# Kernel optimization log

Measured on AMD Instinct MI355X. Metric: run time of the kernel, lower is better.

Reference implementation:

```python
import jax, jax.numpy as jnp
import numpy as np


def _mlp(h, W1, b1, W2, b2):
    # Linear -> ReLU -> Linear
    h = jax.nn.relu(h @ W1 + b1)
    return h @ W2 + b2


def setup_inputs() -> dict:
    key = jax.random.key(0)
    ks = jax.random.split(key, 8)
    N, E, DN, DE, H, O = 50000, 800000, 128, 64, 256, 128
    DIN = DN + DE  # 192
    s1 = 1.0 / np.sqrt(DIN)
    s2 = 1.0 / np.sqrt(H)
    return {
        "x": jax.random.normal(ks[0], (N, DN), dtype=jnp.float32),
        "edge_index": jax.random.randint(ks[1], (2, E), 0, N, dtype=jnp.int32),
        "edge_attr": jax.random.normal(ks[2], (E, DE), dtype=jnp.float32),
        "W1_out": jax.random.normal(ks[3], (DIN, H), dtype=jnp.float32) * s1,
        "b1_out": jnp.zeros((H,), dtype=jnp.float32),
        "W2_out": jax.random.normal(ks[4], (H, O), dtype=jnp.float32) * s2,
        "b2_out": jnp.zeros((O,), dtype=jnp.float32),
        "W1_in": jax.random.normal(ks[5], (DIN, H), dtype=jnp.float32) * s1,
        "b1_in": jnp.zeros((H,), dtype=jnp.float32),
        "W2_in": jax.random.normal(ks[6], (H, O), dtype=jnp.float32) * s2,
        "b2_in": jnp.zeros((O,), dtype=jnp.float32),
    }


def reference(x, edge_index, edge_attr, W1_out, b1_out, W2_out, b2_out,
              W1_in, b1_in, W2_in, b2_in):
    N = x.shape[0]
    row, col = edge_index[0], edge_index[1]
    # Shared gather + concat: [E, d_node + d_edge]
    msg_in = jnp.concatenate([x[col], edge_attr], axis=1)

    # flow_out: edges with row < col. Compute MLP densely, zero masked edges,
    # then scatter-sum -> identical math to masked gather + scatter-sum.
    m_out = (row < col).astype(x.dtype)[:, None]
    flow_out = _mlp(msg_in, W1_out, b1_out, W2_out, b2_out) * m_out
    flow_out = jax.ops.segment_sum(flow_out, row, num_segments=N)

    # flow_in: edges with row > col
    m_in = (row > col).astype(x.dtype)[:, None]
    flow_in = _mlp(msg_in, W1_in, b1_in, W2_in, b2_in) * m_in
    flow_in = jax.ops.segment_sum(flow_in, row, num_segments=N)

    return jnp.concatenate((flow_in, flow_out), axis=1)  # [N, 2*O]
```

## Files before the change

### kernel.cpp

```cpp
#include <hip/hip_runtime.h>
#include <hip/hip_bf16.h>

typedef __attribute__((ext_vector_type(8))) short short8;
typedef __attribute__((ext_vector_type(4))) float f32x4;

#define DN   128
#define DE   64
#define DIN  192
#define HID  256
#define OUTD 128
#define TE   64
#define MSG_LD 200
#define H_LD   264

static __device__ __forceinline__ unsigned short f2b(float f) {
    unsigned int u = __float_as_uint(f);
    u += 0x7fffu + ((u >> 16) & 1u);
    return (unsigned short)(u >> 16);
}

__global__ void pack_all_kernel(const float* __restrict__ W1o, const float* __restrict__ W1i,
                                const float* __restrict__ W2o, const float* __restrict__ W2i,
                                unsigned short* __restrict__ W1po, unsigned short* __restrict__ W1pi,
                                unsigned short* __restrict__ W2po, unsigned short* __restrict__ W2pi) {
    const int S1 = DIN * HID, S2 = HID * OUTD;
    int idx = blockIdx.x * blockDim.x + threadIdx.x;
    const float* W; unsigned short* Wp; int Ncols, j;
    if      (idx < S1)            { W = W1o; Wp = W1po; Ncols = HID;  j = idx; }
    else if (idx < 2*S1)          { W = W1i; Wp = W1pi; Ncols = HID;  j = idx - S1; }
    else if (idx < 2*S1 + S2)     { W = W2o; Wp = W2po; Ncols = OUTD; j = idx - 2*S1; }
    else if (idx < 2*S1 + 2*S2)   { W = W2i; Wp = W2pi; Ncols = OUTD; j = idx - 2*S1 - S2; }
    else return;
    int k = j / Ncols, n = j - k * Ncols;
    Wp[(((k >> 5) * Ncols + n) << 5) + (k & 31)] = f2b(W[j]);
}

__global__ __launch_bounds__(1024)
void partition_kernel(const int* __restrict__ ei, int E,
                      int* __restrict__ cnt,
                      int* __restrict__ list_out, int* __restrict__ list_in) {
    __shared__ int s_wcnt[2][16];
    __shared__ int s_base[2];
    const int tid  = threadIdx.x;
    const int wave = tid >> 6, lane = tid & 63;
    int e = blockIdx.x * blockDim.x + tid;
    bool valid = e < E;
    int r = valid ? ei[e] : 0;
    int c = valid ? ei[E + e] : 0;
    bool po = valid && (r < c);
    bool pi = valid && (r > c);
    unsigned long long mo = __ballot(po);
    unsigned long long mi = __ballot(pi);
    if (lane == 0) { s_wcnt[0][wave] = __popcll(mo); s_wcnt[1][wave] = __popcll(mi); }
    __syncthreads();
    if (tid == 0) {
        int t0 = 0, t1 = 0;
        #pragma unroll
        for (int w = 0; w < 16; ++w) { t0 += s_wcnt[0][w]; t1 += s_wcnt[1][w]; }
        s_base[0] = atomicAdd(&cnt[0], t0);
        s_base[1] = atomicAdd(&cnt[1], t1);
    }
    __syncthreads();
    int woff0 = 0, woff1 = 0;
    for (int w = 0; w < wave; ++w) { woff0 += s_wcnt[0][w]; woff1 += s_wcnt[1][w]; }
    unsigned long long below = (1ull << lane) - 1ull;
    if (po) list_out[s_base[0] + woff0 + __popcll(mo & below)] = e;
    if (pi) list_in [s_base[1] + woff1 + __popcll(mi & below)] = e;
}

__global__ __launch_bounds__(256, 4)
void mlp_scatter_kernel(const float* __restrict__ x,
                        const int* __restrict__ ei,
                        const float* __restrict__ ea,
                        const unsigned short* __restrict__ W1p_out,
                        const unsigned short* __restrict__ W1p_in,
                        const float* __restrict__ b1_out,
                        const float* __restrict__ b1_in,
                        const unsigned short* __restrict__ W2p_out,
                        const unsigned short* __restrict__ W2p_in,
                        const float* __restrict__ b2_out,
                        const float* __restrict__ b2_in,
                        const int* __restrict__ list_out,
                        const int* __restrict__ list_in,
                        const int* __restrict__ cnt,
                        float* __restrict__ out,
                        int E, int nbpb) {
    __shared__ __align__(16) unsigned short s_buf[TE * H_LD];
    __shared__ int s_eid[TE], s_dest[TE], s_col[TE];

    const int branch = (blockIdx.x >= nbpb) ? 1 : 0;
    const int lb = blockIdx.x - branch * nbpb;
    const int count = cnt[branch];
    if (lb * TE >= count) return;
    const int* list            = branch ? list_in : list_out;
    const unsigned short* W1p  = branch ? W1p_in  : W1p_out;
    const float* b1            = branch ? b1_in   : b1_out;
    const unsigned short* W2p  = branch ? W2p_in  : W2p_out;
    const float* b2            = branch ? b2_in   : b2_out;
    const int colbase          = branch ? 0 : OUTD;

    const int tid = threadIdx.x;
    if (tid < TE) {
        int idx = lb * TE + tid;
        int e = (idx < count) ? list[idx] : -1;
        s_eid[tid]  = e;
        s_dest[tid] = (e >= 0) ? ei[e] : -1;
        s_col[tid]  = (e >= 0) ? ei[E + e] : 0;
    }
    __syncthreads();

    {
        const int le  = tid >> 2;
        const int sub = tid & 3;
        const int e   = s_eid[le];
        const long xbase = (long)s_col[le] * 32;
        const long ebase = (long)e * 16;
        #pragma unroll
        for (int j = 0; j < 12; ++j) {
            int q = sub + j * 4;
            float4 v = make_float4(0.f, 0.f, 0.f, 0.f);
            if (e >= 0) {
                if (j < 8) v = reinterpret_cast<const float4*>(x)[xbase + q];
                else       v = reinterpret_cast<const float4*>(ea)[ebase + (q - 32)];
            }
            unsigned int lo = (unsigned int)f2b(v.x) | ((unsigned int)f2b(v.y) << 16);
            unsigned int hi = (unsigned int)f2b(v.z) | ((unsigned int)f2b(v.w) << 16);
            *reinterpret_cast<uint2*>(&s_buf[le * MSG_LD + q * 4]) = make_uint2(lo, hi);
        }
    }
    __syncthreads();

    const int wave = tid >> 6;
    const int lane = tid & 63;
    const int ln   = lane & 15;
    const int quad = lane >> 4;

    f32x4 acc[4][4];
    {
        const int nbase = wave * 64;
        float bias[4];
        #pragma unroll
        for (int t = 0; t < 4; ++t) bias[t] = b1[nbase + t * 16 + ln];
        #pragma unroll
        for (int mt = 0; mt < 4; ++mt)
            #pragma unroll
            for (int t = 0; t < 4; ++t)
                acc[mt][t] = (f32x4){bias[t], bias[t], bias[t], bias[t]};
        #pragma unroll
        for (int kt = 0; kt < DIN / 32; ++kt) {
            short8 a[4], b[4];
            #pragma unroll
            for (int mt = 0; mt < 4; ++mt)
                a[mt] = *reinterpret_cast<const short8*>(
                    &s_buf[(mt * 16 + ln) * MSG_LD + kt * 32 + quad * 8]);
            #pragma unroll
            for (int t = 0; t < 4; ++t)
                b[t] = *reinterpret_cast<const short8*>(
                    &W1p[((kt * HID + nbase + t * 16 + ln) << 5) + quad * 8]);
            #pragma unroll
            for (int mt = 0; mt < 4; ++mt)
                #pragma unroll
                for (int t = 0; t < 4; ++t)
                    acc[mt][t] = __builtin_amdgcn_mfma_f32_16x16x32_bf16(a[mt], b[t], acc[mt][t], 0, 0, 0);
        }
    }
    __syncthreads();

    {
        const int nbase = wave * 64;
        #pragma unroll
        for (int mt = 0; mt < 4; ++mt)
            #pragma unroll
            for (int t = 0; t < 4; ++t) {
                int ncol = nbase + t * 16 + ln;
                #pragma unroll
                for (int r = 0; r < 4; ++r) {
                    int m = mt * 16 + quad * 4 + r;
                    float v = acc[mt][t][r];
                    s_buf[m * H_LD + ncol] = f2b(v > 0.f ? v : 0.f);
                }
            }
    }
    __syncthreads();

    {
        const int nbase = wave * 32;
        float bias2[2];
        #pragma unroll
        for (int t = 0; t < 2; ++t) bias2[t] = b2[nbase + t * 16 + ln];
        f32x4 acc2[4][2];
        #pragma unroll
        for (int mt = 0; mt < 4; ++mt)
            #pragma unroll
            for (int t = 0; t < 2; ++t)
                acc2[mt][t] = (f32x4){bias2[t], bias2[t], bias2[t], bias2[t]};
        #pragma unroll
        for (int kt = 0; kt < HID / 32; ++kt) {
            short8 a[4], b[2];
            #pragma unroll
            for (int mt = 0; mt < 4; ++mt)
                a[mt] = *reinterpret_cast<const short8*>(
                    &s_buf[(mt * 16 + ln) * H_LD + kt * 32 + quad * 8]);
            #pragma unroll
            for (int t = 0; t < 2; ++t)
                b[t] = *reinterpret_cast<const short8*>(
                    &W2p[((kt * OUTD + nbase + t * 16 + ln) << 5) + quad * 8]);
            #pragma unroll
            for (int mt = 0; mt < 4; ++mt)
                #pragma unroll
                for (int t = 0; t < 2; ++t)
                    acc2[mt][t] = __builtin_amdgcn_mfma_f32_16x16x32_bf16(a[mt], b[t], acc2[mt][t], 0, 0, 0);
        }
        #pragma unroll
        for (int mt = 0; mt < 4; ++mt) {
            #pragma unroll
            for (int r = 0; r < 4; ++r) {
                int m = mt * 16 + quad * 4 + r;
                int dest = s_dest[m];
                if (dest >= 0) {
                    float* orow = out + (size_t)dest * (2 * OUTD) + colbase + nbase + ln;
                    atomicAdd(orow,      acc2[mt][0][r]);
                    atomicAdd(orow + 16, acc2[mt][1][r]);
                }
            }
        }
    }
}

extern "C" void kernel_launch(void* const* d_in, const int* in_sizes, int n_in,
                              void* d_out, int out_size, void* d_ws, size_t ws_size,
                              hipStream_t stream) {
    const float* x   = (const float*)d_in[0];
    const int*   ei  = (const int*)d_in[1];
    const float* ea  = (const float*)d_in[2];
    const float* W1o = (const float*)d_in[3];
    const float* b1o = (const float*)d_in[4];
    const float* W2o = (const float*)d_in[5];
    const float* b2o = (const float*)d_in[6];
    const float* W1i = (const float*)d_in[7];
    const float* b1i = (const float*)d_in[8];
    const float* W2i = (const float*)d_in[9];
    const float* b2i = (const float*)d_in[10];
    float* out = (float*)d_out;
    const int E = in_sizes[1] / 2;

    char* ws = (char*)d_ws;
    int* cnt      = (int*)ws;
    int* list_out = (int*)(ws + 256);
    int* list_in  = list_out + E;
    unsigned short* W1po = (unsigned short*)(ws + 256 + (size_t)2 * E * sizeof(int));
    unsigned short* W1pi = W1po + DIN * HID;
    unsigned short* W2po = W1pi + DIN * HID;
    unsigned short* W2pi = W2po + HID * OUTD;

    hipMemsetAsync(d_out, 0, (size_t)out_size * sizeof(float), stream);
    hipMemsetAsync(cnt, 0, 2 * sizeof(int), stream);

    const int packN = 2 * DIN * HID + 2 * HID * OUTD;
    pack_all_kernel<<<(packN + 255) / 256, 256, 0, stream>>>(
        W1o, W1i, W2o, W2i, W1po, W1pi, W2po, W2pi);

    partition_kernel<<<(E + 1023) / 1024, 1024, 0, stream>>>(ei, E, cnt, list_out, list_in);

    const int nbpb = (E + TE - 1) / TE;
    mlp_scatter_kernel<<<2 * nbpb, 256, 0, stream>>>(
        x, ei, ea, W1po, W1pi, b1o, b1i, W2po, W2pi, b2o, b2i,
        list_out, list_in, cnt, out, E, nbpb);
}
```

Measured before the change: 694.9 us.

## Counting-sort edges by destination row and segment-reduce outputs before atomics

Replaces the compacting partition with a histogram, scan and reorder (a counting sort by row) so each direction's edge list is grouped by destination node. The MLP kernel stages its second-layer output in shared memory and does a per-column run-length reduction over consecutive equal destinations, issuing one atomic per run instead of one per edge. This aims to cut global atomic traffic in the scatter. It adds three extra kernels, including a two-block serial scan over N, plus extra atomics on the per-row cursors during reordering.

Result: faster. 660.4 us (-5.0%).

```diff
diff --git a/kernel.cpp b/kernel.cpp
--- a/kernel.cpp
+++ b/kernel.cpp
@@ -12,6 +12,7 @@
 #define TE   64
 #define MSG_LD 200
 #define H_LD   264
+#define OUT_LD 132
 
 static __device__ __forceinline__ unsigned short f2b(float f) {
     unsigned int u = __float_as_uint(f);
@@ -35,37 +36,65 @@
     Wp[(((k >> 5) * Ncols + n) << 5) + (k & 31)] = f2b(W[j]);
 }
 
+__global__ __launch_bounds__(256)
+void part_hist_kernel(const int* __restrict__ ei, int E, int N, int* __restrict__ hist) {
+    int e = blockIdx.x * blockDim.x + threadIdx.x;
+    if (e >= E) return;
+    int r = ei[e], c = ei[E + e];
+    if      (r < c) atomicAdd(&hist[r], 1);
+    else if (r > c) atomicAdd(&hist[N + r], 1);
+}
+
 __global__ __launch_bounds__(1024)
-void partition_kernel(const int* __restrict__ ei, int E,
-                      int* __restrict__ cnt,
-                      int* __restrict__ list_out, int* __restrict__ list_in) {
-    __shared__ int s_wcnt[2][16];
-    __shared__ int s_base[2];
-    const int tid  = threadIdx.x;
-    const int wave = tid >> 6, lane = tid & 63;
-    int e = blockIdx.x * blockDim.x + tid;
-    bool valid = e < E;
-    int r = valid ? ei[e] : 0;
-    int c = valid ? ei[E + e] : 0;
-    bool po = valid && (r < c);
-    bool pi = valid && (r > c);
-    unsigned long long mo = __ballot(po);
-    unsigned long long mi = __ballot(pi);
-    if (lane == 0) { s_wcnt[0][wave] = __popcll(mo); s_wcnt[1][wave] = __popcll(mi); }
-    __syncthreads();
-    if (tid == 0) {
-        int t0 = 0, t1 = 0;
-        #pragma unroll
-        for (int w = 0; w < 16; ++w) { t0 += s_wcnt[0][w]; t1 += s_wcnt[1][w]; }
-        s_base[0] = atomicAdd(&cnt[0], t0);
-        s_base[1] = atomicAdd(&cnt[1], t1);
-    }
-    __syncthreads();
-    int woff0 = 0, woff1 = 0;
-    for (int w = 0; w < wave; ++w) { woff0 += s_wcnt[0][w]; woff1 += s_wcnt[1][w]; }
-    unsigned long long below = (1ull << lane) - 1ull;
-    if (po) list_out[s_base[0] + woff0 + __popcll(mo & below)] = e;
-    if (pi) list_in [s_base[1] + woff1 + __popcll(mi & below)] = e;
+void scan_kernel(const int* __restrict__ hist, int* __restrict__ cursor,
+                 int* __restrict__ cnt, int N) {
+    __shared__ int s_ws[16];
+    __shared__ int s_run;
+    const int tid = threadIdx.x, lane = tid & 63, wv = tid >> 6;
+    const int b = blockIdx.x;
+    const int* h = hist + (size_t)b * N;
+    int* cu = cursor + (size_t)b * N;
+    if (tid == 0) s_run = 0;
+    __syncthreads();
+    for (int base = 0; base < N; base += 1024) {
+        int i = base + tid;
+        int v = (i < N) ? h[i] : 0;
+        int incl = v;
+        #pragma unroll
+        for (int d = 1; d < 64; d <<= 1) {
+            int t = __shfl_up(incl, d, 64);
+            if (lane >= d) incl += t;
+        }
+        if (lane == 63) s_ws[wv] = incl;
+        __syncthreads();
+        if (tid < 16) {
+            int w = s_ws[tid];
+            int wi = w;
+            #pragma unroll
+            for (int d = 1; d < 16; d <<= 1) {
+                int t = __shfl_up(wi, d, 64);
+                if (tid >= d) wi += t;
+            }
+            s_ws[tid] = wi - w;
+        }
+        __syncthreads();
+        int excl = s_run + s_ws[wv] + incl - v;
+        if (i < N) cu[i] = excl;
+        __syncthreads();
+        if (tid == 1023) s_run = excl + v;
+        __syncthreads();
+    }
+    if (tid == 0) cnt[b] = s_run;
+}
+
+__global__ __launch_bounds__(256)
+void reorder_kernel(const int* __restrict__ ei, int E, int N, int* __restrict__ cursor,
+                    int* __restrict__ list_out, int* __restrict__ list_in) {
+    int e = blockIdx.x * blockDim.x + threadIdx.x;
+    if (e >= E) return;
+    int r = ei[e], c = ei[E + e];
+    if      (r < c) { int p = atomicAdd(&cursor[r], 1);            list_out[p] = e; }
+    else if (r > c) { int p = atomicAdd(&cursor[(size_t)N + r], 1); list_in[p] = e; }
 }
 
 __global__ __launch_bounds__(256, 4)
@@ -183,12 +212,12 @@
     }
     __syncthreads();
 
+    f32x4 acc2[4][2];
     {
         const int nbase = wave * 32;
         float bias2[2];
         #pragma unroll
         for (int t = 0; t < 2; ++t) bias2[t] = b2[nbase + t * 16 + ln];
-        f32x4 acc2[4][2];
         #pragma unroll
         for (int mt = 0; mt < 4; ++mt)
             #pragma unroll
@@ -211,19 +240,38 @@
                 for (int t = 0; t < 2; ++t)
                     acc2[mt][t] = __builtin_amdgcn_mfma_f32_16x16x32_bf16(a[mt], b[t], acc2[mt][t], 0, 0, 0);
         }
-        #pragma unroll
-        for (int mt = 0; mt < 4; ++mt) {
-            #pragma unroll
-            for (int r = 0; r < 4; ++r) {
-                int m = mt * 16 + quad * 4 + r;
-                int dest = s_dest[m];
-                if (dest >= 0) {
-                    float* orow = out + (size_t)dest * (2 * OUTD) + colbase + nbase + ln;
-                    atomicAdd(orow,      acc2[mt][0][r]);
-                    atomicAdd(orow + 16, acc2[mt][1][r]);
-                }
+    }
+    __syncthreads();
+
+    float* s_outf = reinterpret_cast<float*>(s_buf);
+    {
+        const int nbase = wave * 32;
+        #pragma unroll
+        for (int mt = 0; mt < 4; ++mt)
+            #pragma unroll
+            for (int t = 0; t < 2; ++t)
+                #pragma unroll
+                for (int r = 0; r < 4; ++r)
+                    s_outf[(mt * 16 + quad * 4 + r) * OUT_LD + nbase + t * 16 + ln] = acc2[mt][t][r];
+    }
+    __syncthreads();
+
+    {
+        const int c  = tid & 127;
+        const int m0 = (tid >> 7) * 32;
+        float run = 0.f;
+        int cur = -1;
+        #pragma unroll 8
+        for (int m = m0; m < m0 + 32; ++m) {
+            int d = s_dest[m];
+            float v = s_outf[m * OUT_LD + c];
+            if (d != cur) {
+                if (cur >= 0) atomicAdd(&out[(size_t)cur * (2 * OUTD) + colbase + c], run);
+                cur = d; run = 0.f;
             }
-        }
+            if (d >= 0) run += v;
+        }
+        if (cur >= 0) atomicAdd(&out[(size_t)cur * (2 * OUTD) + colbase + c], run);
     }
 }
 
@@ -243,24 +291,29 @@
     const float* b2i = (const float*)d_in[10];
     float* out = (float*)d_out;
     const int E = in_sizes[1] / 2;
+    const int N = in_sizes[0] / DN;
 
     char* ws = (char*)d_ws;
     int* cnt      = (int*)ws;
-    int* list_out = (int*)(ws + 256);
+    int* hist     = (int*)(ws + 64);
+    int* cursor   = hist + 2 * (size_t)N;
+    int* list_out = cursor + 2 * (size_t)N;
     int* list_in  = list_out + E;
-    unsigned short* W1po = (unsigned short*)(ws + 256 + (size_t)2 * E * sizeof(int));
+    unsigned short* W1po = (unsigned short*)(list_in + E);
     unsigned short* W1pi = W1po + DIN * HID;
     unsigned short* W2po = W1pi + DIN * HID;
     unsigned short* W2pi = W2po + HID * OUTD;
 
     hipMemsetAsync(d_out, 0, (size_t)out_size * sizeof(float), stream);
-    hipMemsetAsync(cnt, 0, 2 * sizeof(int), stream);
+    hipMemsetAsync(ws, 0, 64 + 2 * (size_t)N * sizeof(int), stream);
 
     const int packN = 2 * DIN * HID + 2 * HID * OUTD;
     pack_all_kernel<<<(packN + 255) / 256, 256, 0, stream>>>(
         W1o, W1i, W2o, W2i, W1po, W1pi, W2po, W2pi);
 
-    partition_kernel<<<(E + 1023) / 1024, 1024, 0, stream>>>(ei, E, cnt, list_out, list_in);
+    part_hist_kernel<<<(E + 255) / 256, 256, 0, stream>>>(ei, E, N, hist);
+    scan_kernel<<<2, 1024, 0, stream>>>(hist, cursor, cnt, N);
+    reorder_kernel<<<(E + 255) / 256, 256, 0, stream>>>(ei, E, N, cursor, list_out, list_in);
 
     const int nbpb = (E + TE - 1) / TE;
     mlp_scatter_kernel<<<2 * nbpb, 256, 0, stream>>>(
```
